# Optimization experiments

Hardware: AMD Instinct MI355X
Metric: run time of the kernel (lower is better)

Reference implementation:

```python
import jax, jax.numpy as jnp
import numpy as np

B, S, H, P, L, O, E = 32, 1024, 256, 96, 200, 200, 64
N_EULER = 4


def setup_inputs() -> dict:
    key = jax.random.key(0)
    ks = jax.random.split(key, 20)
    def w(k, shape, fan_in):
        return jax.random.normal(k, shape, dtype=jnp.float32) / np.float32(np.sqrt(fan_in))
    return {
        'eco_data': jax.random.normal(ks[0], (B, E), dtype=jnp.float32),
        'tran_data': jax.random.normal(ks[1], (B, S, H), dtype=jnp.float32),
        'tran_data_label': jax.random.normal(ks[2], (B, P, 1), dtype=jnp.float32),
        'time_x': jax.random.uniform(ks[3], (B, S, 1), dtype=jnp.float32),
        'time_y': jax.random.uniform(ks[4], (B, P, 1), dtype=jnp.float32),
        'alpha': jnp.ones((1,), dtype=jnp.float32),
        'W_eco': w(ks[5], (E, H), E), 'b_eco': jnp.zeros((H,), jnp.float32),
        'W_in': w(ks[6], (3, H, L), H), 'W_t': w(ks[7], (3, 1, L), 1), 'b_in': jnp.zeros((3, L), jnp.float32),
        'W_f1': w(ks[8], (3, L, O), L), 'b_f1': jnp.zeros((3, O), jnp.float32),
        'W_f2': w(ks[9], (3, O, L), O), 'b_f2': jnp.zeros((3, L), jnp.float32),
        'W_out': w(ks[10], (3, L, H), L), 'b_out': jnp.zeros((3, H), jnp.float32),
        'W_lin': w(ks[11], (H, P), H), 'b_lin': jnp.zeros((P,), jnp.float32),
    }


def reference(eco_data, tran_data, tran_data_label, time_x, time_y, alpha,
              W_eco, b_eco, W_in, W_t, b_in, W_f1, b_f1, W_f2, b_f2,
              W_out, b_out, W_lin, b_lin):
    S_ = tran_data.shape[1]
    # eco_model: linear encoder [B, E] -> [B, H]
    eco_vec = eco_data @ W_eco + b_eco
    # time features over the observed window (concat then slice, per original)
    time_f = jnp.concatenate([time_x, time_y], axis=1)[:, :S_, :]  # [B, S, 1]
    # ODE_RNN for Q/K/V, stacked on k=3: encode -> Euler ODE solve -> readout
    h = jnp.tanh(jnp.einsum('bsh,khl->kbsl', tran_data, W_in)
                 + jnp.einsum('bst,ktl->kbsl', time_f, W_t)
                 + b_in[:, None, None, :])  # [3, B, S, L]
    dt = jnp.float32(1.0 / N_EULER)
    for _ in range(N_EULER):  # fixed-step Euler solve of tanh-MLP vector field
        hid = jnp.tanh(jnp.einsum('kbsl,klo->kbso', h, W_f1) + b_f1[:, None, None, :])
        f = jnp.einsum('kbso,kol->kbsl', hid, W_f2) + b_f2[:, None, None, :]
        h = h + dt * f
    qkv = (jnp.einsum('kbsl,klh->kbsh', h, W_out) + b_out[:, None, None, :]
           + eco_vec[None, :, None, :])  # [3, B, S, H]
    # zero out padded timesteps (last channel == 0 means padding)
    mask = jnp.where(tran_data[:, :, -1] == 0, 0.0, 1.0)[None, :, :, None]
    qkv = qkv * mask
    Q, K, V = qkv[0], qkv[1], qkv[2]
    scale = jnp.float32(1.0 / np.sqrt(H))
    scores = jnp.einsum('bqh,bkh->bqk', Q, K) * scale  # [B, S, S]
    attn = jax.nn.softmax(scores, axis=-1)
    ctx = jnp.einsum('bqk,bkh->bqh', attn, V)  # [B, S, H]
    out = ctx @ W_lin + b_lin  # [B, S, P]
    return out
```

## Files before the change

### kernel.cpp

```cpp
#include <hip/hip_runtime.h>

constexpr int Bc = 32, Sc = 1024, Hc = 256, Pc = 96, Lc = 200, Oc = 200, Ec = 64;
constexpr int Mtot = Bc * Sc;
constexpr float DT = 0.25f;
constexpr int KP = 224;

enum { MODE_ENC = 0, MODE_QKV = 3, MODE_OUT = 4, MODE_BF16OUT = 5 };

typedef short bf16x8 __attribute__((ext_vector_type(8)));
typedef float f32x4 __attribute__((ext_vector_type(4)));
typedef unsigned short u16x8 __attribute__((ext_vector_type(8)));
typedef unsigned int u32x2 __attribute__((ext_vector_type(2)));

__device__ inline unsigned short f2bf(float x) {
    union { float f; unsigned int u; } v; v.f = x;
    unsigned int r = v.u + 0x7FFFu + ((v.u >> 16) & 1u);
    return (unsigned short)(r >> 16);
}
__device__ inline float bf2f(unsigned short x) {
    union { unsigned int u; float f; } v; v.u = ((unsigned int)x) << 16;
    return v.f;
}
__device__ inline float fast_tanh(float x) {
    float e = __expf(2.f * x);
    float r = __frcp_rn(e + 1.f);
    return fmaf(-2.f, r, 1.f);
}
__device__ inline unsigned int cvt_pk_bf16(float a, float b) {
    unsigned int r;
    asm("v_cvt_pk_bf16_f32 %0, %1, %2" : "=v"(r) : "v"(a), "v"(b));
    return r;
}

__global__ __launch_bounds__(256) void eco_kernel(
    const float* __restrict__ eco_data, const float* __restrict__ W_eco,
    const float* __restrict__ b_eco, float* __restrict__ eco_vec)
{
    const int b = blockIdx.x, h = threadIdx.x;
    float acc = b_eco[h];
    #pragma unroll
    for (int e = 0; e < Ec; e++)
        acc = fmaf(eco_data[b * Ec + e], W_eco[(size_t)e * Hc + h], acc);
    eco_vec[(size_t)b * Hc + h] = acc;
}

__global__ void wtrans_all(
    const float* __restrict__ W_in, const float* __restrict__ W_f1,
    const float* __restrict__ W_f2, const float* __restrict__ W_out,
    const float* __restrict__ W_lin,
    unsigned short* __restrict__ WinT, unsigned short* __restrict__ Wf1T,
    unsigned short* __restrict__ Wf2T, unsigned short* __restrict__ WoutT,
    unsigned short* __restrict__ WlinT)
{
    const int z = blockIdx.z;
    const int n = blockIdx.x * 16 + threadIdx.x;
    const int k = blockIdx.y * 16 + threadIdx.y;

    const float* W; unsigned short* WT;
    int K, N, Kpad, Npad;
    if (z < 3)       { W = W_in  + (size_t)z * 256 * 200;       WT = WinT  + (size_t)z * 256 * 256;       K = 256; N = 200; Kpad = 256; Npad = 256; }
    else if (z < 6)  { W = W_f1  + (size_t)(z - 3) * 200 * 200; WT = Wf1T  + (size_t)(z - 3) * 224 * 256; K = 200; N = 200; Kpad = 224; Npad = 256; }
    else if (z < 9)  { W = W_f2  + (size_t)(z - 6) * 200 * 200; WT = Wf2T  + (size_t)(z - 6) * 224 * 256; K = 200; N = 200; Kpad = 224; Npad = 256; }
    else if (z < 12) { W = W_out + (size_t)(z - 9) * 200 * 256; WT = WoutT + (size_t)(z - 9) * 224 * 256; K = 200; N = 256; Kpad = 224; Npad = 256; }
    else             { W = W_lin;                               WT = WlinT;                               K = 256; N =  96; Kpad = 256; Npad = 128; }

    if (n >= Npad || k >= Kpad) return;
    float v = (n < N && k < K) ? W[(size_t)k * N + n] : 0.f;
    WT[(size_t)n * Kpad + k] = f2bf(v);
}

template <int MODE, typename TA>
__global__ __launch_bounds__(256) void mfma_gemm(
    const TA* __restrict__ A, const unsigned short* __restrict__ WT,
    const float* __restrict__ bias, void* __restrict__ Cv,
    int M, int N, int K, int Kpad,
    size_t aStrideZ, size_t wStrideZ, size_t bStrideZ, size_t cStrideZ,
    const float* __restrict__ timev, const float* __restrict__ wtv,
    const float* __restrict__ eco, const float* __restrict__ trandat,
    unsigned short* __restrict__ Ck, unsigned short* __restrict__ Cvt)
{
    constexpr int LDS_S = 40;
    __shared__ unsigned short SM[128 * LDS_S * 2];
    unsigned short* As = SM;
    unsigned short* Bs = SM + 128 * LDS_S;

    const int tid = threadIdx.x;
    const int z = blockIdx.z;
    const int m0 = blockIdx.y * 128;
    const int n0 = blockIdx.x * 128;

    A    += (size_t)z * aStrideZ;
    WT   += (size_t)z * wStrideZ;
    bias += (size_t)z * bStrideZ;
    float* Cf = (float*)Cv + (size_t)z * cStrideZ;
    unsigned short* Cu = (unsigned short*)Cv + (size_t)z * cStrideZ;
    const float* wtp = wtv ? (wtv + (size_t)z * Lc) : nullptr;

    const int lane = tid & 63, wave = tid >> 6;
    const int wm = (wave & 1) * 64, wn = (wave >> 1) * 64;
    const int fm = lane & 15, fq = lane >> 4;

    f32x4 acc[4][4];
    #pragma unroll
    for (int i = 0; i < 4; i++)
        #pragma unroll
        for (int j = 0; j < 4; j++)
            acc[i][j] = (f32x4){0.f, 0.f, 0.f, 0.f};

    for (int k0 = 0; k0 < K; k0 += 32) {
        if (k0) __syncthreads();
        #pragma unroll
        for (int i = 0; i < 4; i++) {
            const int f = i * 256 + tid;
            const int row = f >> 3, kq = f & 7;
            const int k = k0 + kq * 4;
            ushort4 s;
            if constexpr (sizeof(TA) == 4) {
                float4 v = {0.f, 0.f, 0.f, 0.f};
                if (k < K) v = *(const float4*)((const float*)A + (size_t)(m0 + row) * K + k);
                s.x = f2bf(v.x); s.y = f2bf(v.y); s.z = f2bf(v.z); s.w = f2bf(v.w);
            } else {
                s = make_ushort4(0, 0, 0, 0);
                if (k < K) s = *(const ushort4*)((const unsigned short*)A + (size_t)(m0 + row) * K + k);
            }
            *(ushort4*)&As[row * LDS_S + kq * 4] = s;
        }
        #pragma unroll
        for (int i = 0; i < 2; i++) {
            const int f = i * 256 + tid;
            const int row = f >> 2, q = f & 3;
            u16x8 v = *(const u16x8*)(WT + (size_t)(n0 + row) * Kpad + k0 + q * 8);
            *(u16x8*)&Bs[row * LDS_S + q * 8] = v;
        }
        __syncthreads();

        bf16x8 af[4], bfr[4];
        #pragma unroll
        for (int mi = 0; mi < 4; mi++)
            af[mi] = *(const bf16x8*)&As[(wm + mi * 16 + fm) * LDS_S + fq * 8];
        #pragma unroll
        for (int nj = 0; nj < 4; nj++)
            bfr[nj] = *(const bf16x8*)&Bs[(wn + nj * 16 + fm) * LDS_S + fq * 8];
        #pragma unroll
        for (int mi = 0; mi < 4; mi++)
            #pragma unroll
            for (int nj = 0; nj < 4; nj++)
                acc[mi][nj] = __builtin_amdgcn_mfma_f32_16x16x32_bf16(
                    af[mi], bfr[nj], acc[mi][nj], 0, 0, 0);
    }

    if (MODE == MODE_QKV && z == 2) {
        constexpr int BSTR = 136;
        const int bq = m0 >> 10, sq0 = m0 & (Sc - 1);
        const int myhalf = wn >> 6;
        #pragma unroll
        for (int half = 0; half < 2; half++) {
            __syncthreads();
            if (myhalf == half) {
                #pragma unroll
                for (int mi = 0; mi < 4; mi++)
                    #pragma unroll
                    for (int nj = 0; nj < 4; nj++) {
                        const int nn = n0 + wn + nj * 16 + fm;
                        const float bv = bias[nn];
                        const float ev = eco[(size_t)bq * Hc + nn];
                        #pragma unroll
                        for (int r = 0; r < 4; r++) {
                            const int mm = m0 + wm + mi * 16 + fq * 4 + r;
                            float v = acc[mi][nj][r] + bv + ev;
                            if (trandat[(size_t)mm * Hc + (Hc - 1)] == 0.f) v = 0.f;
                            SM[(nj * 16 + fm) * BSTR + wm + mi * 16 + fq * 4 + r] = f2bf(v);
                        }
                    }
            }
            __syncthreads();
            #pragma unroll
            for (int i = 0; i < 4; i++) {
                const int vv = i * 256 + tid;
                const int nl = vv >> 4, vc = vv & 15;
                *(u16x8*)&Cvt[((size_t)bq * Hc + n0 + half * 64 + nl) * Sc + sq0 + vc * 8] =
                    *(const u16x8*)&SM[nl * BSTR + vc * 8];
            }
        }
        return;
    }

    #pragma unroll
    for (int mi = 0; mi < 4; mi++) {
        #pragma unroll
        for (int nj = 0; nj < 4; nj++) {
            const int nn = n0 + wn + nj * 16 + fm;
            if (nn >= N) continue;
            const float bv = (MODE == MODE_BF16OUT) ? 0.f
                           : ((MODE == MODE_ENC && nn >= Lc) ? 0.f : bias[nn]);
            #pragma unroll
            for (int r = 0; r < 4; r++) {
                const int mm = m0 + wm + mi * 16 + fq * 4 + r;
                float v = acc[mi][nj][r] + bv;
                if (MODE == MODE_ENC) {
                    float vv = (nn < Lc) ? fast_tanh(v + timev[mm] * wtp[nn]) : 0.f;
                    Cu[(size_t)mm * N + nn] = f2bf(vv);
                } else if (MODE == MODE_QKV) {
                    v += eco[(size_t)(mm >> 10) * Hc + nn];
                    if (trandat[(size_t)mm * Hc + (Hc - 1)] == 0.f) v = 0.f;
                    if (z == 0)      ((unsigned short*)Cv)[(size_t)mm * Hc + nn] = f2bf(v * 0.0625f);
                    else             Ck[(size_t)mm * Hc + nn] = f2bf(v);
                } else if (MODE == MODE_BF16OUT) {
                    Cu[(size_t)mm * N + nn] = f2bf(v);
                } else {
                    Cf[(size_t)mm * N + nn] = v;
                }
            }
        }
    }
}

__global__ __launch_bounds__(512, 2) void euler_fused(
    unsigned short* __restrict__ hg,
    const unsigned short* __restrict__ W1,
    const unsigned short* __restrict__ W2,
    const float* __restrict__ b1g, const float* __restrict__ b2g)
{
    constexpr int HS = 232;
    constexpr int WS = 40;
    extern __shared__ unsigned short lds[];
    unsigned short* hs  = lds;
    unsigned short* wsb[2] = { lds + 29696, lds + 38656 };
    unsigned short* hcb[2] = { lds + 47616, lds + 52736 };
    float* bs = (float*)(lds + 57856);

    const int tid = threadIdx.x;
    const int z = blockIdx.y;
    const int m0 = blockIdx.x * 128;
    unsigned short* hrow = hg + ((size_t)z * Mtot + m0) * KP;
    const unsigned short* W1z = W1 + (size_t)z * 256 * KP;
    const unsigned short* W2z = W2 + (size_t)z * 256 * KP;

    const int lane = tid & 63, w = tid >> 6;
    const int wm = (w & 3) * 32, wn = (w >> 2) * 112;
    const int fm = lane & 15, fq = lane >> 4;

    const int sr = tid >> 2, sq = tid & 3;
    const bool s2 = (tid < 384);

    if (tid < 448) {
        float v;
        if (tid < 224) v = (tid < Oc) ? b1g[z * Oc + tid] : 0.f;
        else { const int t = tid - 224; v = (t < Lc) ? b2g[z * Lc + t] : 0.f; }
        bs[tid] = v;
    }

    u16x8 pr0, pr1;
    pr0 = *(const u16x8*)&W1z[sr * KP + sq * 8];
    if (s2) pr1 = *(const u16x8*)&W1z[(sr + 128) * KP + sq * 8];

    #pragma unroll
    for (int i = 0; i < 7; i++) {
        const int f = i * 512 + tid;
        const int r = f / 28, c = (f % 28) * 8;
        *(u16x8*)&hs[r * HS + c] = *(const u16x8*)&hrow[(size_t)r * KP + c];
    }

    for (int it = 0; it < 4; it++) {
        __syncthreads();
        *(u16x8*)&wsb[0][sr * WS + sq * 8] = pr0;
        if (s2) *(u16x8*)&wsb[0][(sr + 128) * WS + sq * 8] = pr1;
        pr0 = *(const u16x8*)&W1z[sr * KP + 32 + sq * 8];
        if (s2) pr1 = *(const u16x8*)&W1z[(sr + 128) * KP + 32 + sq * 8];
        __syncthreads();

        f32x4 acc[2][7];
        #pragma unroll
        for (int mi = 0; mi < 2; mi++)
            #pragma unroll
            for (int nj = 0; nj < 7; nj++)
                acc[mi][nj] = (f32x4){0.f, 0.f, 0.f, 0.f};

        for (int k = 0; k < 7; k++) {
            if (k < 6) {
                unsigned short* wb = wsb[(k + 1) & 1];
                *(u16x8*)&wb[sr * WS + sq * 8] = pr0;
                if (s2) *(u16x8*)&wb[(sr + 128) * WS + sq * 8] = pr1;
                const unsigned short* src = (k + 2 < 7) ? (W1z + (k + 2) * 32) : W2z;
                pr0 = *(const u16x8*)&src[sr * KP + sq * 8];
                if (s2) pr1 = *(const u16x8*)&src[(sr + 128) * KP + sq * 8];
            }
            const unsigned short* wr = wsb[k & 1];
            bf16x8 af[2], bfr[7];
            #pragma unroll
            for (int mi = 0; mi < 2; mi++)
                af[mi] = *(const bf16x8*)&hs[(wm + mi * 16 + fm) * HS + k * 32 + fq * 8];
            #pragma unroll
            for (int nj = 0; nj < 7; nj++)
                bfr[nj] = *(const bf16x8*)&wr[(wn + nj * 16 + fm) * WS + fq * 8];
            #pragma unroll
            for (int mi = 0; mi < 2; mi++)
                #pragma unroll
                for (int nj = 0; nj < 7; nj++)
                    acc[mi][nj] = __builtin_amdgcn_mfma_f32_16x16x32_bf16(
                        bfr[nj], af[mi], acc[mi][nj], 0, 0, 0);
            __syncthreads();
        }

        unsigned int hidp[2][7][2];
        #pragma unroll
        for (int nj = 0; nj < 7; nj++) {
            const f32x4 b1v = *(const f32x4*)&bs[wn + nj * 16 + fq * 4];
            #pragma unroll
            for (int mi = 0; mi < 2; mi++) {
                const float t0 = fast_tanh(acc[mi][nj][0] + b1v[0]);
                const float t1 = fast_tanh(acc[mi][nj][1] + b1v[1]);
                const float t2 = fast_tanh(acc[mi][nj][2] + b1v[2]);
                const float t3 = fast_tanh(acc[mi][nj][3] + b1v[3]);
                hidp[mi][nj][0] = cvt_pk_bf16(t0, t1);
                hidp[mi][nj][1] = cvt_pk_bf16(t2, t3);
            }
        }

        {
            *(u16x8*)&wsb[0][sr * WS + sq * 8] = pr0;
            if (s2) *(u16x8*)&wsb[0][(sr + 128) * WS + sq * 8] = pr1;
            pr0 = *(const u16x8*)&W2z[sr * KP + 32 + sq * 8];
            if (s2) pr1 = *(const u16x8*)&W2z[(sr + 128) * KP + 32 + sq * 8];
            #pragma unroll
            for (int t2 = 0; t2 < 2; t2++) {
                const int c0 = t2 * 16;
                if (c0 >= wn && c0 < wn + 112) {
                    const int nj = (c0 - wn) >> 4;
                    #pragma unroll
                    for (int mi = 0; mi < 2; mi++) {
                        u32x2 p; p[0] = hidp[mi][nj][0]; p[1] = hidp[mi][nj][1];
                        *(u32x2*)&hcb[0][(wm + mi * 16 + fm) * WS + t2 * 16 + fq * 4] = p;
                    }
                }
            }
        }
        __syncthreads();

        f32x4 fac[2][7];
        #pragma unroll
        for (int mi = 0; mi < 2; mi++)
            #pragma unroll
            for (int nj = 0; nj < 7; nj++)
                fac[mi][nj] = (f32x4){0.f, 0.f, 0.f, 0.f};

        for (int k = 0; k < 7; k++) {
            if (k < 6) {
                unsigned short* wb = wsb[(k + 1) & 1];
                unsigned short* hb = hcb[(k + 1) & 1];
                *(u16x8*)&wb[sr * WS + sq * 8] = pr0;
                if (s2) *(u16x8*)&wb[(sr + 128) * WS + sq * 8] = pr1;
                if (k + 2 < 7) {
                    pr0 = *(const u16x8*)&W2z[sr * KP + (k + 2) * 32 + sq * 8];
                    if (s2) pr1 = *(const u16x8*)&W2z[(sr + 128) * KP + (k + 2) * 32 + sq * 8];
                } else if (it != 3) {
                    pr0 = *(const u16x8*)&W1z[sr * KP + sq * 8];
                    if (s2) pr1 = *(const u16x8*)&W1z[(sr + 128) * KP + sq * 8];
                }
                #pragma unroll
                for (int t2 = 0; t2 < 2; t2++) {
                    const int c0 = (k + 1) * 32 + t2 * 16;
                    if (c0 >= wn && c0 < wn + 112) {
                        const int nj = (c0 - wn) >> 4;
                        #pragma unroll
                        for (int mi = 0; mi < 2; mi++) {
                            u32x2 p; p[0] = hidp[mi][nj][0]; p[1] = hidp[mi][nj][1];
                            *(u32x2*)&hb[(wm + mi * 16 + fm) * WS + t2 * 16 + fq * 4] = p;
                        }
                    }
                }
            }
            const unsigned short* wr = wsb[k & 1];
            const unsigned short* hr = hcb[k & 1];
            bf16x8 af2[2], bf2[7];
            #pragma unroll
            for (int mi = 0; mi < 2; mi++)
                af2[mi] = *(const bf16x8*)&hr[(wm + mi * 16 + fm) * WS + fq * 8];
            #pragma unroll
            for (int nj = 0; nj < 7; nj++)
                bf2[nj] = *(const bf16x8*)&wr[(wn + nj * 16 + fm) * WS + fq * 8];
            #pragma unroll
            for (int mi = 0; mi < 2; mi++)
                #pragma unroll
                for (int nj = 0; nj < 7; nj++)
                    fac[mi][nj] = __builtin_amdgcn_mfma_f32_16x16x32_bf16(
                        bf2[nj], af2[mi], fac[mi][nj], 0, 0, 0);
            __syncthreads();
        }

        #pragma unroll
        for (int nj = 0; nj < 7; nj++) {
            const int n = wn + nj * 16 + fq * 4;
            const f32x4 b2v = *(const f32x4*)&bs[224 + n];
            #pragma unroll
            for (int mi = 0; mi < 2; mi++) {
                const int m = wm + mi * 16 + fm;
                const ushort4 hv = *(const ushort4*)&hs[m * HS + n];
                const float v0 = bf2f(hv.x) + DT * (fac[mi][nj][0] + b2v[0]);
                const float v1 = bf2f(hv.y) + DT * (fac[mi][nj][1] + b2v[1]);
                const float v2 = bf2f(hv.z) + DT * (fac[mi][nj][2] + b2v[2]);
                const float v3 = bf2f(hv.w) + DT * (fac[mi][nj][3] + b2v[3]);
                u32x2 p; p[0] = cvt_pk_bf16(v0, v1); p[1] = cvt_pk_bf16(v2, v3);
                *(u32x2*)&hs[m * HS + n] = p;
            }
        }
    }

    __syncthreads();
    #pragma unroll
    for (int i = 0; i < 7; i++) {
        const int f = i * 512 + tid;
        const int r = f / 28, c = (f % 28) * 8;
        *(u16x8*)&hrow[(size_t)r * KP + c] = *(const u16x8*)&hs[r * HS + c];
    }
}

__global__ __launch_bounds__(512) void flash_attn(
    const unsigned short* __restrict__ Qb, const unsigned short* __restrict__ Kb,
    const unsigned short* __restrict__ VT, unsigned short* __restrict__ ctx)
{
    constexpr int QS = 264;
    constexpr int KS = 264;
    constexpr int VS = 72;
    constexpr int PS = 72;
    extern __shared__ unsigned short lds[];
    unsigned short* qs = lds;
    unsigned short* ks = lds + 128 * QS;
    unsigned short* vs = lds + 128 * QS + 64 * KS;
    unsigned short* ps = lds + 128 * QS + 64 * KS + 256 * VS;

    const int tid = threadIdx.x;
    const int b = blockIdx.y, q0 = blockIdx.x * 128;
    const int lane = tid & 63, w = tid >> 6;
    const int fm = lane & 15, fq = lane >> 4;
    unsigned short* psw = ps + w * 16 * PS;

    const unsigned short* Qp = Qb + (size_t)b * Sc * Hc;
    const unsigned short* Kp = Kb + (size_t)b * Sc * Hc;
    const unsigned short* Vp = VT + (size_t)b * Hc * Sc;

    #pragma unroll
    for (int i = 0; i < 8; i++) {
        const int v = i * 512 + tid;
        *(u16x8*)&qs[(v >> 5) * QS + (v & 31) * 8] =
            *(const u16x8*)&Qp[(size_t)(q0 + (v >> 5)) * Hc + (v & 31) * 8];
    }

    f32x4 of[16];
    #pragma unroll
    for (int nj = 0; nj < 16; nj++) of[nj] = (f32x4){0.f, 0.f, 0.f, 0.f};
    float lrun[4] = {0.f, 0.f, 0.f, 0.f};

    for (int c = 0; c < 16; c++) {
        __syncthreads();
        const int s0 = c * 64;
        #pragma unroll
        for (int i = 0; i < 4; i++) {
            const int v = i * 512 + tid;
            *(u16x8*)&ks[(v >> 5) * KS + (v & 31) * 8] =
                *(const u16x8*)&Kp[(size_t)(s0 + (v >> 5)) * Hc + (v & 31) * 8];
            *(u16x8*)&vs[(v >> 3) * VS + (v & 7) * 8] =
                *(const u16x8*)&Vp[(size_t)(v >> 3) * Sc + s0 + (v & 7) * 8];
        }
        __syncthreads();

        f32x4 sc[4];
        #pragma unroll
        for (int nj = 0; nj < 4; nj++) sc[nj] = (f32x4){0.f, 0.f, 0.f, 0.f};
        #pragma unroll
        for (int kc = 0; kc < 8; kc++) {
            const bf16x8 aq = *(const bf16x8*)&qs[(w * 16 + fm) * QS + kc * 32 + fq * 8];
            #pragma unroll
            for (int nj = 0; nj < 4; nj++) {
                const bf16x8 bk = *(const bf16x8*)&ks[(nj * 16 + fm) * KS + kc * 32 + fq * 8];
                sc[nj] = __builtin_amdgcn_mfma_f32_16x16x32_bf16(aq, bk, sc[nj], 0, 0, 0);
            }
        }

        float rsum[4] = {0.f, 0.f, 0.f, 0.f};
        #pragma unroll
        for (int nj = 0; nj < 4; nj++)
            #pragma unroll
            for (int r = 0; r < 4; r++) {
                const float p = __expf(sc[nj][r]);
                rsum[r] += p;
                psw[(fq * 4 + r) * PS + nj * 16 + fm] = f2bf(p);
            }
        #pragma unroll
        for (int r = 0; r < 4; r++) {
            float s = rsum[r];
            #pragma unroll
            for (int o = 8; o > 0; o >>= 1) s += __shfl_xor(s, o, 64);
            lrun[r] += s;
        }

        #pragma unroll
        for (int t = 0; t < 2; t++) {
            const bf16x8 ap = *(const bf16x8*)&psw[fm * PS + t * 32 + fq * 8];
            #pragma unroll
            for (int nj = 0; nj < 16; nj++) {
                const bf16x8 bv = *(const bf16x8*)&vs[(nj * 16 + fm) * VS + t * 32 + fq * 8];
                of[nj] = __builtin_amdgcn_mfma_f32_16x16x32_bf16(ap, bv, of[nj], 0, 0, 0);
            }
        }
    }

    float inv[4];
    #pragma unroll
    for (int r = 0; r < 4; r++) inv[r] = __frcp_rn(lrun[r]);
    #pragma unroll
    for (int nj = 0; nj < 16; nj++)
        #pragma unroll
        for (int r = 0; r < 4; r++)
            ctx[((size_t)b * Sc + q0 + w * 16 + fq * 4 + r) * Hc + nj * 16 + fm] =
                f2bf(of[nj][r] * inv[r]);
}

extern "C" void kernel_launch(void* const* d_in, const int* in_sizes, int n_in,
                              void* d_out, int out_size, void* d_ws, size_t ws_size,
                              hipStream_t stream)
{
    const float* eco_data = (const float*)d_in[0];
    const float* tran     = (const float*)d_in[1];
    const float* time_x   = (const float*)d_in[3];
    const float* W_eco    = (const float*)d_in[6];
    const float* b_eco    = (const float*)d_in[7];
    const float* W_in     = (const float*)d_in[8];
    const float* W_t      = (const float*)d_in[9];
    const float* b_in     = (const float*)d_in[10];
    const float* W_f1     = (const float*)d_in[11];
    const float* b_f1     = (const float*)d_in[12];
    const float* W_f2     = (const float*)d_in[13];
    const float* b_f2     = (const float*)d_in[14];
    const float* W_out    = (const float*)d_in[15];
    const float* b_out    = (const float*)d_in[16];
    const float* W_lin    = (const float*)d_in[17];
    const float* b_lin    = (const float*)d_in[18];
    float* out = (float*)d_out;

    float* eco_vec = (float*)d_ws;
    unsigned short* hpad = (unsigned short*)(eco_vec + 8192);
    unsigned short* Qb = hpad + (size_t)3 * Mtot * KP;
    unsigned short* Kb = Qb + (size_t)Mtot * Hc;
    unsigned short* VT = Kb + (size_t)Mtot * Hc;
    unsigned short* P  = VT + (size_t)Mtot * Hc;
    unsigned short* WinT  = P + (size_t)Mtot * Sc;
    unsigned short* Wf1T  = WinT  + (size_t)3 * 256 * 256;
    unsigned short* Wf2T  = Wf1T  + (size_t)3 * 256 * KP;
    unsigned short* WoutT = Wf2T  + (size_t)3 * 256 * KP;
    unsigned short* WlinT = WoutT + (size_t)3 * 256 * KP;
    unsigned short* ctxb = hpad;

    constexpr int EULER_LDS = 57856 * 2 + 448 * 4;
    static_assert(EULER_LDS == 117504, "euler lds");
    hipFuncSetAttribute((const void*)euler_fused,
                        hipFuncAttributeMaxDynamicSharedMemorySize, EULER_LDS);
    constexpr int FLASH_LDS = (128 * 264 + 64 * 264 + 256 * 72 + 8 * 16 * 72) * 2;
    static_assert(FLASH_LDS == 156672, "flash lds");
    hipFuncSetAttribute((const void*)flash_attn,
                        hipFuncAttributeMaxDynamicSharedMemorySize, FLASH_LDS);

    eco_kernel<<<Bc, Hc, 0, stream>>>(eco_data, W_eco, b_eco, eco_vec);

    wtrans_all<<<dim3(16, 16, 13), dim3(16, 16), 0, stream>>>(
        W_in, W_f1, W_f2, W_out, W_lin, WinT, Wf1T, Wf2T, WoutT, WlinT);

    const dim3 blk(256);

    mfma_gemm<MODE_ENC, float><<<dim3(2, 256, 3), blk, 0, stream>>>(
        tran, WinT, b_in, hpad, Mtot, KP, Hc, 256,
        0, 65536, Lc, (size_t)Mtot * KP, time_x, W_t, nullptr, nullptr, nullptr, nullptr);

    euler_fused<<<dim3(Mtot / 128, 3), 512, EULER_LDS, stream>>>(
        hpad, Wf1T, Wf2T, b_f1, b_f2);

    mfma_gemm<MODE_QKV, unsigned short><<<dim3(2, 256, 3), blk, 0, stream>>>(
        hpad, WoutT, b_out, Qb, Mtot, Hc, KP, KP,
        (size_t)Mtot * KP, 57344, Hc, 0, nullptr, nullptr, eco_vec, tran, Kb, VT);

    flash_attn<<<dim3(8, 32), 512, FLASH_LDS, stream>>>(Qb, Kb, VT, ctxb);

    mfma_gemm<MODE_OUT, unsigned short><<<dim3(1, 256, 1), blk, 0, stream>>>(
        ctxb, WlinT, b_lin, out, Mtot, Pc, Hc, 256,
        0, 0, 0, 0, nullptr, nullptr, nullptr, nullptr, nullptr, nullptr);
}
```

Before: 481.3 us.

## Double-buffer LDS tiles with register prefetch in MFMA GEMM

The GEMM main loop now uses two LDS buffers. Global loads for the next K-slice go into registers before the current slice's MFMAs, and are written to the other buffer afterwards, so only one barrier per iteration is needed and load latency overlaps compute. This doubles LDS use and adds prefetch registers, which may lower occupancy. The k<K bounds guard was removed and the trip count is now K/32, so a K that is not a multiple of 32 would drop its tail columns.

```diff
diff --git a/kernel.cpp b/kernel.cpp
--- a/kernel.cpp
+++ b/kernel.cpp
@@ -80,9 +80,8 @@
     unsigned short* __restrict__ Ck, unsigned short* __restrict__ Cvt)
 {
     constexpr int LDS_S = 40;
-    __shared__ unsigned short SM[128 * LDS_S * 2];
-    unsigned short* As = SM;
-    unsigned short* Bs = SM + 128 * LDS_S;
+    constexpr int HALF = 128 * LDS_S;
+    __shared__ unsigned short SM[4 * HALF];
 
     const int tid = threadIdx.x;
     const int z = blockIdx.z;
@@ -107,46 +106,77 @@
         for (int j = 0; j < 4; j++)
             acc[i][j] = (f32x4){0.f, 0.f, 0.f, 0.f};
 
-    for (int k0 = 0; k0 < K; k0 += 32) {
-        if (k0) __syncthreads();
+    float4  paf[4];
+    ushort4 pau[4];
+    u16x8   pb[2];
+
+    auto LOAD = [&](int k0) {
         #pragma unroll
         for (int i = 0; i < 4; i++) {
             const int f = i * 256 + tid;
             const int row = f >> 3, kq = f & 7;
-            const int k = k0 + kq * 4;
-            ushort4 s;
-            if constexpr (sizeof(TA) == 4) {
-                float4 v = {0.f, 0.f, 0.f, 0.f};
-                if (k < K) v = *(const float4*)((const float*)A + (size_t)(m0 + row) * K + k);
-                s.x = f2bf(v.x); s.y = f2bf(v.y); s.z = f2bf(v.z); s.w = f2bf(v.w);
-            } else {
-                s = make_ushort4(0, 0, 0, 0);
-                if (k < K) s = *(const ushort4*)((const unsigned short*)A + (size_t)(m0 + row) * K + k);
-            }
-            *(ushort4*)&As[row * LDS_S + kq * 4] = s;
+            if constexpr (sizeof(TA) == 4)
+                paf[i] = *(const float4*)((const float*)A + (size_t)(m0 + row) * K + k0 + kq * 4);
+            else
+                pau[i] = *(const ushort4*)((const unsigned short*)A + (size_t)(m0 + row) * K + k0 + kq * 4);
         }
         #pragma unroll
         for (int i = 0; i < 2; i++) {
             const int f = i * 256 + tid;
             const int row = f >> 2, q = f & 3;
-            u16x8 v = *(const u16x8*)(WT + (size_t)(n0 + row) * Kpad + k0 + q * 8);
-            *(u16x8*)&Bs[row * LDS_S + q * 8] = v;
-        }
+            pb[i] = *(const u16x8*)(WT + (size_t)(n0 + row) * Kpad + k0 + q * 8);
+        }
+    };
+    auto STORE = [&](int buf) {
+        unsigned short* Asd = SM + buf * 2 * HALF;
+        unsigned short* Bsd = Asd + HALF;
+        #pragma unroll
+        for (int i = 0; i < 4; i++) {
+            const int f = i * 256 + tid;
+            const int row = f >> 3, kq = f & 7;
+            ushort4 s;
+            if constexpr (sizeof(TA) == 4) {
+                s.x = f2bf(paf[i].x); s.y = f2bf(paf[i].y);
+                s.z = f2bf(paf[i].z); s.w = f2bf(paf[i].w);
+            } else {
+                s = pau[i];
+            }
+            *(ushort4*)&Asd[row * LDS_S + kq * 4] = s;
+        }
+        #pragma unroll
+        for (int i = 0; i < 2; i++) {
+            const int f = i * 256 + tid;
+            const int row = f >> 2, q = f & 3;
+            *(u16x8*)&Bsd[row * LDS_S + q * 8] = pb[i];
+        }
+    };
+
+    const int nk = K >> 5;
+    LOAD(0);
+    STORE(0);
+
+    for (int ki = 0; ki < nk; ki++) {
         __syncthreads();
+        const unsigned short* Asr = SM + (ki & 1) * 2 * HALF;
+        const unsigned short* Bsr = Asr + HALF;
+
+        if (ki + 1 < nk) LOAD((ki + 1) * 32);
 
         bf16x8 af[4], bfr[4];
         #pragma unroll
         for (int mi = 0; mi < 4; mi++)
-            af[mi] = *(const bf16x8*)&As[(wm + mi * 16 + fm) * LDS_S + fq * 8];
+            af[mi] = *(const bf16x8*)&Asr[(wm + mi * 16 + fm) * LDS_S + fq * 8];
         #pragma unroll
         for (int nj = 0; nj < 4; nj++)
-            bfr[nj] = *(const bf16x8*)&Bs[(wn + nj * 16 + fm) * LDS_S + fq * 8];
+            bfr[nj] = *(const bf16x8*)&Bsr[(wn + nj * 16 + fm) * LDS_S + fq * 8];
         #pragma unroll
         for (int mi = 0; mi < 4; mi++)
             #pragma unroll
             for (int nj = 0; nj < 4; nj++)
                 acc[mi][nj] = __builtin_amdgcn_mfma_f32_16x16x32_bf16(
                     af[mi], bfr[nj], acc[mi][nj], 0, 0, 0);
+
+        if (ki + 1 < nk) STORE((ki + 1) & 1);
     }
 
     if (MODE == MODE_QKV && z == 2) {
```

Result: faster. 458.8 us (-4.7%).
